# Performance work log

Hardware: AMD Instinct MI355X
Metric: run time of the kernel (lower is better)

Reference implementation:

```python
import math
import jax, jax.numpy as jnp
import numpy as np

D_MODEL = 128
NUM_HEADS = 8
FACTOR = 5


def setup_inputs() -> dict:
    key = jax.random.key(0)
    ks = jax.random.split(key, 9)
    B, L, dm = 2, 4096, D_MODEL
    s = 1.0 / math.sqrt(dm)
    return {
        "x": jax.random.normal(ks[0], (B, L, dm), dtype=jnp.float32),
        "Wq": jax.random.normal(ks[1], (dm, dm), dtype=jnp.float32) * s,
        "bq": jnp.zeros((dm,), jnp.float32),
        "Wk": jax.random.normal(ks[2], (dm, dm), dtype=jnp.float32) * s,
        "bk": jnp.zeros((dm,), jnp.float32),
        "Wv": jax.random.normal(ks[3], (dm, dm), dtype=jnp.float32) * s,
        "bv": jnp.zeros((dm,), jnp.float32),
        "Wo": jax.random.normal(ks[4], (dm, dm), dtype=jnp.float32) * s,
        "bo": jnp.zeros((dm,), jnp.float32),
    }


def reference(x, Wq, bq, Wk, bk, Wv, bv, Wo, bo):
    B, L, dm = x.shape
    H = NUM_HEADS
    D = dm // H
    inv_sqrt_d = 1.0 / math.sqrt(D)

    def split_heads(t):  # [B,L,dm] -> [B,H,L,D]
        return t.reshape(B, L, H, D).transpose(0, 2, 1, 3)

    Q = split_heads(x @ Wq + bq)
    K = split_heads(x @ Wk + bk)
    V = split_heads(x @ Wv + bv)

    # sample_k = min(L_K, int(log(L_K) * factor)); L is static under jit
    sample_k = min(L, int(math.log(L) * FACTOR))

    # _prob_QK: full scores, per-query stable exp, mean over queries, top-k keys
    scores_full = jnp.einsum("bhqd,bhkd->bhqk", Q, K) * inv_sqrt_d  # [B,H,L,L]
    m = jnp.max(scores_full, axis=-1, keepdims=True)
    e = jnp.exp(scores_full - m)
    mean_attn = jnp.mean(e, axis=2)  # [B,H,L_K]
    _, idx = jax.lax.top_k(mean_attn, sample_k)  # [B,H,sample_k]

    # gather sampled keys/values along the key axis
    Ks = jnp.take_along_axis(K, idx[..., None], axis=2)  # [B,H,s,D]
    Vs = jnp.take_along_axis(V, idx[..., None], axis=2)

    attn = jax.nn.softmax(jnp.einsum("bhqd,bhsd->bhqs", Q, Ks) * inv_sqrt_d, axis=-1)
    out = jnp.einsum("bhqs,bhsd->bhqd", attn, Vs)  # [B,H,L,D]
    out = out.transpose(0, 2, 1, 3).reshape(B, L, dm)
    return out @ Wo + bo
```

## Files before the change

### kernel.cpp

```cpp
#include <hip/hip_runtime.h>
#include <hip/hip_bf16.h>

#define L 4096
#define DM 128
#define NH 8
#define HD 16
#define NBH 16
#define SK 41
#define NSPLIT 4
#define QSCALE 0.36067376022224085f

typedef __attribute__((ext_vector_type(8))) short s16x8;
typedef __attribute__((ext_vector_type(4))) float f32x4;

__device__ __forceinline__ float bf2f(unsigned short h){ return __uint_as_float(((unsigned)h)<<16); }
__device__ __forceinline__ unsigned short f2bf(float f){
  unsigned u = __float_as_uint(f);
  u += 0x7FFFu + ((u>>16)&1u);
  return (unsigned short)(u>>16);
}
__device__ __forceinline__ float fast_exp2(float x){
  float r;
  asm("v_exp_f32 %0, %1" : "=v"(r) : "v"(x));
  return r;
}

__global__ __launch_bounds__(256) void prep(
    const float* __restrict__ x,
    const float* __restrict__ Wq, const float* __restrict__ Wk,
    const float* __restrict__ Wv, const float* __restrict__ Wo,
    unsigned short* __restrict__ Xh, unsigned short* __restrict__ Xl,
    unsigned short* __restrict__ Wph, unsigned short* __restrict__ Wpl)
{
  const int t = threadIdx.x;
  const int blk = blockIdx.x;
  if (blk < 1024){
    const long base = (long)blk*1024 + t*4;
    float4 v = *(const float4*)(x + base);
    unsigned short h[4], lo[4];
    h[0]=f2bf(v.x); lo[0]=f2bf(v.x - bf2f(h[0]));
    h[1]=f2bf(v.y); lo[1]=f2bf(v.y - bf2f(h[1]));
    h[2]=f2bf(v.z); lo[2]=f2bf(v.z - bf2f(h[2]));
    h[3]=f2bf(v.w); lo[3]=f2bf(v.w - bf2f(h[3]));
    *(uint2*)(Xh+base) = *(uint2*)h;
    *(uint2*)(Xl+base) = *(uint2*)lo;
  } else {
    const int e = (blk-1024)*256 + t;
    const int p = e >> 14;
    const int idx = e & 16383;
    const int j = idx & 7;
    const int f = idx >> 3;
    const int n = f & 127;
    const int kcg = f >> 7;
    const int k = (kcg>>1)*16 + (kcg&1)*8 + j;
    const float* W = (p==0)?Wq:((p==1)?Wk:((p==2)?Wv:Wo));
    const float v = W[k*128 + n];
    const unsigned short h = f2bf(v);
    Wph[e] = h;
    Wpl[e] = f2bf(v - bf2f(h));
  }
}

__global__ __launch_bounds__(256) void proj_mfma(
    const unsigned short* __restrict__ Xh, const unsigned short* __restrict__ Xl,
    const unsigned short* __restrict__ Wph, const unsigned short* __restrict__ Wpl,
    const float* __restrict__ bq, const float* __restrict__ bk, const float* __restrict__ bv,
    unsigned short* __restrict__ Qh, unsigned short* __restrict__ Ql,
    unsigned short* __restrict__ Kh, unsigned short* __restrict__ Kl,
    float* __restrict__ Vo)
{
  const int p = blockIdx.y;
  const float* __restrict__ bias = (p==0)?bq:((p==1)?bk:bv);
  __shared__ __align__(16) unsigned short wh[16384];
  __shared__ __align__(16) unsigned short wl[16384];
  const int t = threadIdx.x;
  {
    const uint4* gh = (const uint4*)(Wph + (long)p*16384);
    const uint4* gl = (const uint4*)(Wpl + (long)p*16384);
    uint4* sh = (uint4*)wh; uint4* sl = (uint4*)wl;
#pragma unroll
    for (int i=0;i<8;++i){ sh[t + i*256] = gh[t + i*256]; sl[t + i*256] = gl[t + i*256]; }
  }
  __syncthreads();
  const int w = t>>6, l = t&63;
  const int lc = l&15, g = l>>4;
  const int mbase = blockIdx.x*256 + w*64;
  f32x4 acc[4][8];
#pragma unroll
  for (int mt=0;mt<4;++mt)
#pragma unroll
    for (int nt=0;nt<8;++nt){ acc[mt][nt][0]=0.f; acc[mt][nt][1]=0.f; acc[mt][nt][2]=0.f; acc[mt][nt][3]=0.f; }
  const unsigned short* __restrict__ Asrc = (g<2)? Xh : Xl;
  const int koff = (g&1)*8;
  for (int kc=0; kc<8; ++kc){
    s16x8 a[4];
#pragma unroll
    for (int mt=0;mt<4;++mt)
      a[mt] = *(const s16x8*)(Asrc + ((long)(mbase + mt*16 + lc))*128 + kc*16 + koff);
#pragma unroll
    for (int nt=0;nt<8;++nt){
      const int fi = (kc*2+(g&1))*128 + nt*16 + lc;
      s16x8 b1 = ((const s16x8*)wh)[fi];
      s16x8 b2 = ((const s16x8*)wl)[fi];
#pragma unroll
      for (int mt=0;mt<4;++mt){
        acc[mt][nt] = __builtin_amdgcn_mfma_f32_16x16x32_bf16(a[mt], b1, acc[mt][nt], 0,0,0);
        acc[mt][nt] = __builtin_amdgcn_mfma_f32_16x16x32_bf16(a[mt], b2, acc[mt][nt], 0,0,0);
      }
    }
  }
#pragma unroll
  for (int nt=0;nt<8;++nt){
    const float bb = bias[nt*16 + lc];
#pragma unroll
    for (int mt=0;mt<4;++mt){
#pragma unroll
      for (int r=0;r<4;++r){
        const int row = mbase + mt*16 + g*4 + r;
        float v = acc[mt][nt][r] + bb;
        const int b = row>>12, li = row&4095;
        const long o = (((long)(b*NH + nt))*L + li)*HD + lc;
        if (p==2){
          Vo[o] = v;
        } else {
          if (p==0) v *= QSCALE;
          const unsigned short h = f2bf(v);
          const unsigned short lo2 = f2bf(v - bf2f(h));
          if (p==0){ Qh[o]=h; Ql[o]=lo2; } else { Kh[o]=h; Kl[o]=lo2; }
        }
      }
    }
  }
}

__global__ __launch_bounds__(256) void rowmax_k(
    const unsigned short* __restrict__ Qh, const unsigned short* __restrict__ Ql,
    const unsigned short* __restrict__ Kh, const unsigned short* __restrict__ Kl,
    float* __restrict__ mpart)
{
  const int bh = blockIdx.y, qt = blockIdx.x, ks = blockIdx.z;
  const int t = threadIdx.x, w = t>>6, l = t&63;
  const int half = (l>>4)&1, part = l>>5, lc = l&15;
  s16x8 aq[4];
  {
    const unsigned short* Qsrc = part ? Ql : Qh;
#pragma unroll
    for (int m=0;m<4;++m){
      const int row = qt*256 + w*64 + m*16 + lc;
      aq[m] = *(const s16x8*)(Qsrc + (((long)bh*L + row)*HD) + half*8);
    }
  }
  f32x4 fz; fz[0]=0.f; fz[1]=0.f; fz[2]=0.f; fz[3]=0.f;
  f32x4 rmax[4];
#pragma unroll
  for (int m=0;m<4;++m){ rmax[m][0]=rmax[m][1]=rmax[m][2]=rmax[m][3]=-3.4e38f; }
  const unsigned short* khp = Kh + ((long)bh*L + ks*1024 + lc)*HD + half*8;
  const unsigned short* klp = Kl + ((long)bh*L + ks*1024 + lc)*HD + half*8;
  s16x8 nb1 = *(const s16x8*)khp;
  s16x8 nb2 = *(const s16x8*)klp;
  for (int kk=0; kk<64; ++kk){
    s16x8 b1 = nb1, b2 = nb2;
    if (kk < 63){
      nb1 = *(const s16x8*)(khp + (kk+1)*16*HD);
      nb2 = *(const s16x8*)(klp + (kk+1)*16*HD);
    }
#pragma unroll
    for (int m=0;m<4;++m){
      f32x4 acc = __builtin_amdgcn_mfma_f32_16x16x32_bf16(aq[m], b2, fz, 0,0,0);
      acc = __builtin_amdgcn_mfma_f32_16x16x32_bf16(aq[m], b1, acc, 0,0,0);
#pragma unroll
      for (int r=0;r<4;++r) rmax[m][r] = fmaxf(rmax[m][r], acc[r]);
    }
  }
#pragma unroll
  for (int m=0;m<4;++m){
#pragma unroll
    for (int r=0;r<4;++r){
      float v = rmax[m][r];
      v = fmaxf(v, __shfl_xor(v, 1));
      v = fmaxf(v, __shfl_xor(v, 2));
      v = fmaxf(v, __shfl_xor(v, 4));
      v = fmaxf(v, __shfl_xor(v, 8));
      rmax[m][r] = v;
    }
  }
  if (lc == 0){
    const int q4 = l>>4;
#pragma unroll
    for (int m=0;m<4;++m){
#pragma unroll
      for (int r=0;r<4;++r){
        const int row = qt*256 + w*64 + m*16 + q4*4 + r;
        mpart[((long)ks*NBH + bh)*L + row] = rmax[m][r];
      }
    }
  }
}

__global__ __launch_bounds__(256) void mreduce(
    const float* __restrict__ mpart, float* __restrict__ wq)
{
  const int i = blockIdx.x*256 + threadIdx.x;
  float m = -3.4e38f;
#pragma unroll
  for (int p=0;p<NSPLIT;++p) m = fmaxf(m, mpart[(long)p*NBH*L + i]);
  wq[i] = fast_exp2(-m);
}

__global__ __launch_bounds__(256) void colexp_k(
    const unsigned short* __restrict__ Kh, const unsigned short* __restrict__ Kl,
    const unsigned short* __restrict__ Qh, const unsigned short* __restrict__ Ql,
    const float* __restrict__ wq, float* __restrict__ cspart)
{
  const int bh = blockIdx.y, kt = blockIdx.x, qs = blockIdx.z;
  const int t = threadIdx.x, w = t>>6, l = t&63;
  const int half = (l>>4)&1, part = l>>5, lc = l&15;
  s16x8 ak[4];
  {
    const unsigned short* Ksrc = part ? Kl : Kh;
#pragma unroll
    for (int m=0;m<4;++m){
      const int key = kt*256 + w*64 + m*16 + lc;
      ak[m] = *(const s16x8*)(Ksrc + (((long)bh*L + key)*HD) + half*8);
    }
  }
  f32x4 fz; fz[0]=0.f; fz[1]=0.f; fz[2]=0.f; fz[3]=0.f;
  f32x4 csum[4];
#pragma unroll
  for (int m=0;m<4;++m){ csum[m][0]=0.f; csum[m][1]=0.f; csum[m][2]=0.f; csum[m][3]=0.f; }
  const unsigned short* qhp = Qh + ((long)bh*L + qs*1024 + lc)*HD + half*8;
  const unsigned short* qlp = Ql + ((long)bh*L + qs*1024 + lc)*HD + half*8;
  const float* wg = wq + (long)bh*L + qs*1024 + lc;
  s16x8 nb1 = *(const s16x8*)qhp;
  s16x8 nb2 = *(const s16x8*)qlp;
  float nw = *wg;
  for (int kk=0; kk<64; ++kk){
    s16x8 b1 = nb1, b2 = nb2;
    const float wv = nw;
    if (kk < 63){
      nb1 = *(const s16x8*)(qhp + (kk+1)*16*HD);
      nb2 = *(const s16x8*)(qlp + (kk+1)*16*HD);
      nw  = wg[(kk+1)*16];
    }
#pragma unroll
    for (int m=0;m<4;++m){
      f32x4 acc = __builtin_amdgcn_mfma_f32_16x16x32_bf16(ak[m], b2, fz, 0,0,0);
      acc = __builtin_amdgcn_mfma_f32_16x16x32_bf16(ak[m], b1, acc, 0,0,0);
#pragma unroll
      for (int r=0;r<4;++r)
        csum[m][r] = fmaf(fast_exp2(acc[r]), wv, csum[m][r]);
    }
  }
#pragma unroll
  for (int m=0;m<4;++m){
#pragma unroll
    for (int r=0;r<4;++r){
      float v = csum[m][r];
      v += __shfl_xor(v, 1);
      v += __shfl_xor(v, 2);
      v += __shfl_xor(v, 4);
      v += __shfl_xor(v, 8);
      csum[m][r] = v;
    }
  }
  if (lc == 0){
    const int k4 = l>>4;
#pragma unroll
    for (int m=0;m<4;++m){
#pragma unroll
      for (int r=0;r<4;++r){
        const int key = kt*256 + w*64 + m*16 + k4*4 + r;
        cspart[((long)qs*NBH + bh)*L + key] = csum[m][r];
      }
    }
  }
}

__global__ __launch_bounds__(256) void csreduce(
    const float* __restrict__ cspart, float* __restrict__ cs)
{
  const int gid = blockIdx.x*256 + threadIdx.x;
  const long i4 = (long)gid*4;
  float4 s = {0.f,0.f,0.f,0.f};
#pragma unroll
  for (int p=0;p<NSPLIT;++p){
    float4 v = *(const float4*)(cspart + (long)p*NBH*L + i4);
    s.x += v.x; s.y += v.y; s.z += v.z; s.w += v.w;
  }
  *(float4*)(cs + i4) = s;
}

__global__ __launch_bounds__(256) void topk_gather(
    const float* __restrict__ cs,
    const unsigned short* __restrict__ Kh, const unsigned short* __restrict__ Kl,
    const float* __restrict__ V,
    float* __restrict__ Ks, float* __restrict__ Vs)
{
  const int bh = blockIdx.x;
  const int t = threadIdx.x;
  __shared__ float vals[4096];
  __shared__ unsigned hist[2048];
  __shared__ unsigned suf[256];
  __shared__ int meta[4];
  __shared__ int sel[SK];
  __shared__ int sorted[SK];
  __shared__ int tiei[4096];

  for (int i=t; i<1024; i+=256)
    *(float4*)&vals[i*4] = *(const float4*)(cs + (long)bh*L + i*4);
  __syncthreads();

  int target = SK;
  unsigned B1 = 0, P2 = 0, T = 0;
#pragma unroll
  for (int pass=0; pass<3; ++pass){
    const int nb = (pass<2) ? 2048 : 1024;
    const int chunk = nb >> 8;
    for (int i=t;i<nb;i+=256) hist[i]=0u;
    __syncthreads();
    for (int i=t;i<4096;i+=256){
      const unsigned u = __float_as_uint(vals[i]);
      bool ok; int bk;
      if (pass==0){ ok = true;              bk = (int)(u>>21); }
      else if (pass==1){ ok = ((u>>21)==B1); bk = (int)((u>>10)&0x7FFu); }
      else { ok = ((u>>10)==P2);            bk = (int)(u&0x3FFu); }
      if (ok) atomicAdd(&hist[bk], 1u);
    }
    __syncthreads();
    {
      unsigned c=0;
#pragma unroll
      for (int b=0;b<8;++b) if (b<chunk) c += hist[t*chunk+b];
      suf[t]=c;
    }
    __syncthreads();
    for (int off=1; off<256; off<<=1){
      unsigned add = (t+off<256)? suf[t+off] : 0u;
      __syncthreads();
      suf[t] += add;
      __syncthreads();
    }
    {
      const unsigned mysuf = suf[t];
      const unsigned nxt = (t==255)?0u:suf[t+1];
      if (mysuf >= (unsigned)target && nxt < (unsigned)target){
        unsigned running = nxt;
        for (int b=t*chunk+chunk-1; b>=t*chunk; --b){
          const unsigned h = hist[b];
          if (running + h >= (unsigned)target){ meta[0]=b; meta[1]=(int)running; break; }
          running += h;
        }
      }
    }
    __syncthreads();
    const unsigned B = (unsigned)meta[0];
    target -= meta[1];
    if (pass==0) B1 = B;
    else if (pass==1) P2 = (B1<<11)|B;
    else T = (P2<<10)|B;
    __syncthreads();
  }
  if (t==0){ meta[2]=0; meta[3]=0; }
  __syncthreads();
  for (int i=t;i<4096;i+=256){
    const unsigned u = __float_as_uint(vals[i]);
    if (u > T){ int p = atomicAdd(&meta[2],1); sel[p]=i; }
    else if (u == T){ int p = atomicAdd(&meta[3],1); tiei[p]=i; }
  }
  __syncthreads();
  const int ngt = meta[2];
  const int ntie = meta[3];
  for (int j=t; j<ntie; j+=256){
    const int x = tiei[j];
    int rk=0;
    for (int k=0;k<ntie;++k) rk += (tiei[k] < x);
    if (rk < target) sel[ngt+rk] = x;
  }
  __syncthreads();
  if (t<SK){
    int x=sel[t]; int rk=0;
    for (int j=0;j<SK;++j) rk += (sel[j]<x);
    sorted[rk]=x;
  }
  __syncthreads();
  for (int i=t;i<SK*HD;i+=256){
    const int j=i>>4, dd=i&15;
    const int key=sorted[j];
    const long src=((long)bh*L+key)*HD+dd;
    Ks[(long)bh*SK*HD+i]=bf2f(Kh[src])+bf2f(Kl[src]);
    Vs[(long)bh*SK*HD+i]=V[src];
  }
}

__global__ __launch_bounds__(256) void sattn(
    const unsigned short* __restrict__ Qh, const unsigned short* __restrict__ Ql,
    const float* __restrict__ Ks, const float* __restrict__ Vs,
    unsigned short* __restrict__ AOh, unsigned short* __restrict__ AOl)
{
  const int bh = blockIdx.y, qb = blockIdx.x;
  const int t = threadIdx.x;
  __shared__ float ks[SK*HD], vs[SK*HD];
  for (int i=t; i<SK*HD; i+=256){
    ks[i] = Ks[(long)bh*SK*HD + i];
    vs[i] = Vs[(long)bh*SK*HD + i];
  }
  __syncthreads();
  const int q = qb*256 + t;
  const long qo = ((long)bh*L + q)*HD;
  float qv[16];
  {
    s16x8 h0 = *(const s16x8*)(Qh+qo);
    s16x8 h1 = *(const s16x8*)(Qh+qo+8);
    s16x8 l0 = *(const s16x8*)(Ql+qo);
    s16x8 l1 = *(const s16x8*)(Ql+qo+8);
#pragma unroll
    for (int d=0; d<8; ++d){
      qv[d]   = bf2f((unsigned short)h0[d]) + bf2f((unsigned short)l0[d]);
      qv[d+8] = bf2f((unsigned short)h1[d]) + bf2f((unsigned short)l1[d]);
    }
  }
  float mrun = -3.4e38f, lrun = 0.f, out[16];
#pragma unroll
  for (int d=0; d<16; ++d) out[d] = 0.f;
  for (int j=0; j<SK; ++j){
    float4 k0 = *(const float4*)&ks[j*HD+0];
    float4 k1 = *(const float4*)&ks[j*HD+4];
    float4 k2 = *(const float4*)&ks[j*HD+8];
    float4 k3 = *(const float4*)&ks[j*HD+12];
    float s = qv[0]*k0.x;
    s = fmaf(qv[1],k0.y,s); s = fmaf(qv[2],k0.z,s); s = fmaf(qv[3],k0.w,s);
    s = fmaf(qv[4],k1.x,s); s = fmaf(qv[5],k1.y,s); s = fmaf(qv[6],k1.z,s); s = fmaf(qv[7],k1.w,s);
    s = fmaf(qv[8],k2.x,s); s = fmaf(qv[9],k2.y,s); s = fmaf(qv[10],k2.z,s); s = fmaf(qv[11],k2.w,s);
    s = fmaf(qv[12],k3.x,s); s = fmaf(qv[13],k3.y,s); s = fmaf(qv[14],k3.z,s); s = fmaf(qv[15],k3.w,s);
    if (s > mrun){
      const float c = fast_exp2(mrun - s);
      lrun *= c;
#pragma unroll
      for (int d=0; d<16; ++d) out[d] *= c;
      mrun = s;
    }
    const float p = fast_exp2(s - mrun);
    lrun += p;
    float4 v0 = *(const float4*)&vs[j*HD+0];
    float4 v1 = *(const float4*)&vs[j*HD+4];
    float4 v2 = *(const float4*)&vs[j*HD+8];
    float4 v3 = *(const float4*)&vs[j*HD+12];
    out[0]=fmaf(p,v0.x,out[0]); out[1]=fmaf(p,v0.y,out[1]); out[2]=fmaf(p,v0.z,out[2]); out[3]=fmaf(p,v0.w,out[3]);
    out[4]=fmaf(p,v1.x,out[4]); out[5]=fmaf(p,v1.y,out[5]); out[6]=fmaf(p,v1.z,out[6]); out[7]=fmaf(p,v1.w,out[7]);
    out[8]=fmaf(p,v2.x,out[8]); out[9]=fmaf(p,v2.y,out[9]); out[10]=fmaf(p,v2.z,out[10]); out[11]=fmaf(p,v2.w,out[11]);
    out[12]=fmaf(p,v3.x,out[12]); out[13]=fmaf(p,v3.y,out[13]); out[14]=fmaf(p,v3.z,out[14]); out[15]=fmaf(p,v3.w,out[15]);
  }
  const float inv = 1.f / lrun;
  const int b = bh>>3, h = bh&7;
  const long row = (long)b*L + q;
  unsigned short hv[16], lv[16];
#pragma unroll
  for (int d=0; d<16; ++d){
    const float v = out[d]*inv;
    hv[d] = f2bf(v);
    lv[d] = f2bf(v - bf2f(hv[d]));
  }
  unsigned short* oh = AOh + row*DM + h*HD;
  unsigned short* ol = AOl + row*DM + h*HD;
  *(uint4*)(oh)   = *(uint4*)(hv);
  *(uint4*)(oh+8) = *(uint4*)(hv+8);
  *(uint4*)(ol)   = *(uint4*)(lv);
  *(uint4*)(ol+8) = *(uint4*)(lv+8);
}

__global__ __launch_bounds__(256) void outproj_mfma(
    const unsigned short* __restrict__ AOh, const unsigned short* __restrict__ AOl,
    const unsigned short* __restrict__ Wph, const unsigned short* __restrict__ Wpl,
    const float* __restrict__ bo, float* __restrict__ out)
{
  __shared__ __align__(16) unsigned short wh[16384];
  __shared__ __align__(16) unsigned short wl[16384];
  const int t = threadIdx.x;
  {
    const uint4* gh = (const uint4*)(Wph + (long)3*16384);
    const uint4* gl = (const uint4*)(Wpl + (long)3*16384);
    uint4* sh = (uint4*)wh; uint4* sl = (uint4*)wl;
#pragma unroll
    for (int i=0;i<8;++i){ sh[t + i*256] = gh[t + i*256]; sl[t + i*256] = gl[t + i*256]; }
  }
  __syncthreads();
  const int w = t>>6, l = t&63;
  const int lc = l&15, g = l>>4;
  const int mbase = blockIdx.x*256 + w*64;
  f32x4 acc[4][8];
#pragma unroll
  for (int mt=0;mt<4;++mt)
#pragma unroll
    for (int nt=0;nt<8;++nt){ acc[mt][nt][0]=0.f; acc[mt][nt][1]=0.f; acc[mt][nt][2]=0.f; acc[mt][nt][3]=0.f; }
  const unsigned short* __restrict__ Asrc = (g<2)? AOh : AOl;
  const int koff = (g&1)*8;
  for (int kc=0; kc<8; ++kc){
    s16x8 a[4];
#pragma unroll
    for (int mt=0;mt<4;++mt)
      a[mt] = *(const s16x8*)(Asrc + ((long)(mbase + mt*16 + lc))*128 + kc*16 + koff);
#pragma unroll
    for (int nt=0;nt<8;++nt){
      const int fi = (kc*2+(g&1))*128 + nt*16 + lc;
      s16x8 b1 = ((const s16x8*)wh)[fi];
      s16x8 b2 = ((const s16x8*)wl)[fi];
#pragma unroll
      for (int mt=0;mt<4;++mt){
        acc[mt][nt] = __builtin_amdgcn_mfma_f32_16x16x32_bf16(a[mt], b1, acc[mt][nt], 0,0,0);
        acc[mt][nt] = __builtin_amdgcn_mfma_f32_16x16x32_bf16(a[mt], b2, acc[mt][nt], 0,0,0);
      }
    }
  }
#pragma unroll
  for (int nt=0;nt<8;++nt){
    const float bb = bo[nt*16 + lc];
#pragma unroll
    for (int mt=0;mt<4;++mt){
#pragma unroll
      for (int r=0;r<4;++r){
        const int row = mbase + mt*16 + g*4 + r;
        out[(long)row*DM + nt*16 + lc] = acc[mt][nt][r] + bb;
      }
    }
  }
}

extern "C" void kernel_launch(void* const* d_in, const int* in_sizes, int n_in,
                              void* d_out, int out_size, void* d_ws, size_t ws_size,
                              hipStream_t stream)
{
  const float* x  = (const float*)d_in[0];
  const float* Wq = (const float*)d_in[1];
  const float* bq = (const float*)d_in[2];
  const float* Wk = (const float*)d_in[3];
  const float* bk = (const float*)d_in[4];
  const float* Wv = (const float*)d_in[5];
  const float* bv = (const float*)d_in[6];
  const float* Wo = (const float*)d_in[7];
  const float* bo = (const float*)d_in[8];
  float* out = (float*)d_out;

  char* wsp = (char*)d_ws;
  size_t o = 0;
  auto alloc = [&](size_t bytes)->char*{
    char* p = wsp + o; o += (bytes + 255) & ~(size_t)255; return p;
  };
  unsigned short* Qh = (unsigned short*)alloc((size_t)NBH*L*HD*2);
  unsigned short* Ql = (unsigned short*)alloc((size_t)NBH*L*HD*2);
  unsigned short* Kh = (unsigned short*)alloc((size_t)NBH*L*HD*2);
  unsigned short* Kl = (unsigned short*)alloc((size_t)NBH*L*HD*2);
  float* Vv    = (float*)alloc((size_t)NBH*L*HD*4);
  float* mpart = (float*)alloc((size_t)NSPLIT*NBH*L*4);
  float* cspart= (float*)alloc((size_t)NSPLIT*NBH*L*4);
  float* csv   = (float*)alloc((size_t)NBH*L*4);
  float* wqv   = (float*)alloc((size_t)NBH*L*4);
  float* Ks    = (float*)alloc((size_t)NBH*SK*HD*4);
  float* Vs    = (float*)alloc((size_t)NBH*SK*HD*4);
  unsigned short* Xh  = (unsigned short*)alloc((size_t)2*L*DM*2);
  unsigned short* Xl  = (unsigned short*)alloc((size_t)2*L*DM*2);
  unsigned short* AOh = (unsigned short*)alloc((size_t)2*L*DM*2);
  unsigned short* AOl = (unsigned short*)alloc((size_t)2*L*DM*2);
  unsigned short* Wph = (unsigned short*)alloc((size_t)4*16384*2);
  unsigned short* Wpl = (unsigned short*)alloc((size_t)4*16384*2);

  prep<<<1280,256,0,stream>>>(x,Wq,Wk,Wv,Wo,Xh,Xl,Wph,Wpl);
  proj_mfma<<<dim3(32,3),256,0,stream>>>(Xh,Xl,Wph,Wpl,bq,bk,bv,Qh,Ql,Kh,Kl,Vv);
  rowmax_k<<<dim3(16,16,NSPLIT),256,0,stream>>>(Qh,Ql,Kh,Kl,mpart);
  mreduce<<<NBH*L/256,256,0,stream>>>(mpart,wqv);
  colexp_k<<<dim3(16,16,NSPLIT),256,0,stream>>>(Kh,Kl,Qh,Ql,wqv,cspart);
  csreduce<<<NBH*L/1024,256,0,stream>>>(cspart,csv);
  topk_gather<<<16,256,0,stream>>>(csv,Kh,Kl,Vv,Ks,Vs);
  sattn<<<dim3(16,16),256,0,stream>>>(Qh,Ql,Ks,Vs,AOh,AOl);
  outproj_mfma<<<32,256,0,stream>>>(AOh,AOl,Wph,Wpl,bo,out);
}
```

Baseline: 160.2 us.

## Raise parallelism across kernels and fold column-sum reduction into top-k

Doubles the key/query split count in the rowmax and colexp kernels (NSPLIT 4→8) and unrolls their loops by two with explicit double-buffered loads. Halves rows per block in the projection and output GEMMs to double their grid sizes. Splits each query across two threads in sampled attention and merges the two partial softmax states with shuffles. Removes the separate csreduce kernel by summing partials inside topk_gather, trading one launch for more reads in a 16-block kernel. The mreduce kernel (not shown) is assumed to loop over NSPLIT.

```diff
diff --git a/kernel.cpp b/kernel.cpp
--- a/kernel.cpp
+++ b/kernel.cpp
@@ -7,7 +7,9 @@
 #define HD 16
 #define NBH 16
 #define SK 41
-#define NSPLIT 4
+#define NSPLIT 8
+#define SLICE (L/NSPLIT)
+#define KK (SLICE/16)
 #define QSCALE 0.36067376022224085f
 
 typedef __attribute__((ext_vector_type(8))) short s16x8;
@@ -84,18 +86,18 @@
   __syncthreads();
   const int w = t>>6, l = t&63;
   const int lc = l&15, g = l>>4;
-  const int mbase = blockIdx.x*256 + w*64;
-  f32x4 acc[4][8];
-#pragma unroll
-  for (int mt=0;mt<4;++mt)
+  const int mbase = blockIdx.x*128 + w*32;
+  f32x4 acc[2][8];
+#pragma unroll
+  for (int mt=0;mt<2;++mt)
 #pragma unroll
     for (int nt=0;nt<8;++nt){ acc[mt][nt][0]=0.f; acc[mt][nt][1]=0.f; acc[mt][nt][2]=0.f; acc[mt][nt][3]=0.f; }
   const unsigned short* __restrict__ Asrc = (g<2)? Xh : Xl;
   const int koff = (g&1)*8;
   for (int kc=0; kc<8; ++kc){
-    s16x8 a[4];
-#pragma unroll
-    for (int mt=0;mt<4;++mt)
+    s16x8 a[2];
+#pragma unroll
+    for (int mt=0;mt<2;++mt)
       a[mt] = *(const s16x8*)(Asrc + ((long)(mbase + mt*16 + lc))*128 + kc*16 + koff);
 #pragma unroll
     for (int nt=0;nt<8;++nt){
@@ -103,7 +105,7 @@
       s16x8 b1 = ((const s16x8*)wh)[fi];
       s16x8 b2 = ((const s16x8*)wl)[fi];
 #pragma unroll
-      for (int mt=0;mt<4;++mt){
+      for (int mt=0;mt<2;++mt){
         acc[mt][nt] = __builtin_amdgcn_mfma_f32_16x16x32_bf16(a[mt], b1, acc[mt][nt], 0,0,0);
         acc[mt][nt] = __builtin_amdgcn_mfma_f32_16x16x32_bf16(a[mt], b2, acc[mt][nt], 0,0,0);
       }
@@ -113,7 +115,7 @@
   for (int nt=0;nt<8;++nt){
     const float bb = bias[nt*16 + lc];
 #pragma unroll
-    for (int mt=0;mt<4;++mt){
+    for (int mt=0;mt<2;++mt){
 #pragma unroll
       for (int r=0;r<4;++r){
         const int row = mbase + mt*16 + g*4 + r;
@@ -154,20 +156,26 @@
   f32x4 rmax[4];
 #pragma unroll
   for (int m=0;m<4;++m){ rmax[m][0]=rmax[m][1]=rmax[m][2]=rmax[m][3]=-3.4e38f; }
-  const unsigned short* khp = Kh + ((long)bh*L + ks*1024 + lc)*HD + half*8;
-  const unsigned short* klp = Kl + ((long)bh*L + ks*1024 + lc)*HD + half*8;
-  s16x8 nb1 = *(const s16x8*)khp;
-  s16x8 nb2 = *(const s16x8*)klp;
-  for (int kk=0; kk<64; ++kk){
-    s16x8 b1 = nb1, b2 = nb2;
-    if (kk < 63){
-      nb1 = *(const s16x8*)(khp + (kk+1)*16*HD);
-      nb2 = *(const s16x8*)(klp + (kk+1)*16*HD);
-    }
-#pragma unroll
-    for (int m=0;m<4;++m){
-      f32x4 acc = __builtin_amdgcn_mfma_f32_16x16x32_bf16(aq[m], b2, fz, 0,0,0);
-      acc = __builtin_amdgcn_mfma_f32_16x16x32_bf16(aq[m], b1, acc, 0,0,0);
+  const unsigned short* khp = Kh + ((long)bh*L + ks*SLICE + lc)*HD + half*8;
+  const unsigned short* klp = Kl + ((long)bh*L + ks*SLICE + lc)*HD + half*8;
+  s16x8 A1 = *(const s16x8*)khp;
+  s16x8 A2 = *(const s16x8*)klp;
+  for (int kk=0; kk<KK; kk+=2){
+    s16x8 B1 = *(const s16x8*)(khp + (kk+1)*256);
+    s16x8 B2 = *(const s16x8*)(klp + (kk+1)*256);
+#pragma unroll
+    for (int m=0;m<4;++m){
+      f32x4 acc = __builtin_amdgcn_mfma_f32_16x16x32_bf16(aq[m], A2, fz, 0,0,0);
+      acc = __builtin_amdgcn_mfma_f32_16x16x32_bf16(aq[m], A1, acc, 0,0,0);
+#pragma unroll
+      for (int r=0;r<4;++r) rmax[m][r] = fmaxf(rmax[m][r], acc[r]);
+    }
+    A1 = *(const s16x8*)(khp + (kk+2)*256);
+    A2 = *(const s16x8*)(klp + (kk+2)*256);
+#pragma unroll
+    for (int m=0;m<4;++m){
+      f32x4 acc = __builtin_amdgcn_mfma_f32_16x16x32_bf16(aq[m], B2, fz, 0,0,0);
+      acc = __builtin_amdgcn_mfma_f32_16x16x32_bf16(aq[m], B1, acc, 0,0,0);
 #pragma unroll
       for (int r=0;r<4;++r) rmax[m][r] = fmaxf(rmax[m][r], acc[r]);
     }
@@ -228,27 +236,34 @@
   f32x4 csum[4];
 #pragma unroll
   for (int m=0;m<4;++m){ csum[m][0]=0.f; csum[m][1]=0.f; csum[m][2]=0.f; csum[m][3]=0.f; }
-  const unsigned short* qhp = Qh + ((long)bh*L + qs*1024 + lc)*HD + half*8;
-  const unsigned short* qlp = Ql + ((long)bh*L + qs*1024 + lc)*HD + half*8;
-  const float* wg = wq + (long)bh*L + qs*1024 + lc;
-  s16x8 nb1 = *(const s16x8*)qhp;
-  s16x8 nb2 = *(const s16x8*)qlp;
-  float nw = *wg;
-  for (int kk=0; kk<64; ++kk){
-    s16x8 b1 = nb1, b2 = nb2;
-    const float wv = nw;
-    if (kk < 63){
-      nb1 = *(const s16x8*)(qhp + (kk+1)*16*HD);
-      nb2 = *(const s16x8*)(qlp + (kk+1)*16*HD);
-      nw  = wg[(kk+1)*16];
-    }
-#pragma unroll
-    for (int m=0;m<4;++m){
-      f32x4 acc = __builtin_amdgcn_mfma_f32_16x16x32_bf16(ak[m], b2, fz, 0,0,0);
-      acc = __builtin_amdgcn_mfma_f32_16x16x32_bf16(ak[m], b1, acc, 0,0,0);
+  const unsigned short* qhp = Qh + ((long)bh*L + qs*SLICE + lc)*HD + half*8;
+  const unsigned short* qlp = Ql + ((long)bh*L + qs*SLICE + lc)*HD + half*8;
+  const float* wg = wq + (long)bh*L + qs*SLICE + lc;
+  s16x8 A1 = *(const s16x8*)qhp;
+  s16x8 A2 = *(const s16x8*)qlp;
+  float WA = wg[0];
+  for (int kk=0; kk<KK; kk+=2){
+    s16x8 B1 = *(const s16x8*)(qhp + (kk+1)*256);
+    s16x8 B2 = *(const s16x8*)(qlp + (kk+1)*256);
+    float WB = wg[(kk+1)*16];
+#pragma unroll
+    for (int m=0;m<4;++m){
+      f32x4 acc = __builtin_amdgcn_mfma_f32_16x16x32_bf16(ak[m], A2, fz, 0,0,0);
+      acc = __builtin_amdgcn_mfma_f32_16x16x32_bf16(ak[m], A1, acc, 0,0,0);
 #pragma unroll
       for (int r=0;r<4;++r)
-        csum[m][r] = fmaf(fast_exp2(acc[r]), wv, csum[m][r]);
+        csum[m][r] = fmaf(fast_exp2(acc[r]), WA, csum[m][r]);
+    }
+    A1 = *(const s16x8*)(qhp + (kk+2)*256);
+    A2 = *(const s16x8*)(qlp + (kk+2)*256);
+    WA = wg[(kk+2)*16];
+#pragma unroll
+    for (int m=0;m<4;++m){
+      f32x4 acc = __builtin_amdgcn_mfma_f32_16x16x32_bf16(ak[m], B2, fz, 0,0,0);
+      acc = __builtin_amdgcn_mfma_f32_16x16x32_bf16(ak[m], B1, acc, 0,0,0);
+#pragma unroll
+      for (int r=0;r<4;++r)
+        csum[m][r] = fmaf(fast_exp2(acc[r]), WB, csum[m][r]);
     }
   }
 #pragma unroll
@@ -276,22 +291,8 @@
   }
 }
 
-__global__ __launch_bounds__(256) void csreduce(
-    const float* __restrict__ cspart, float* __restrict__ cs)
-{
-  const int gid = blockIdx.x*256 + threadIdx.x;
-  const long i4 = (long)gid*4;
-  float4 s = {0.f,0.f,0.f,0.f};
-#pragma unroll
-  for (int p=0;p<NSPLIT;++p){
-    float4 v = *(const float4*)(cspart + (long)p*NBH*L + i4);
-    s.x += v.x; s.y += v.y; s.z += v.z; s.w += v.w;
-  }
-  *(float4*)(cs + i4) = s;
-}
-
 __global__ __launch_bounds__(256) void topk_gather(
-    const float* __restrict__ cs,
+    const float* __restrict__ cspart,
     const unsigned short* __restrict__ Kh, const unsigned short* __restrict__ Kl,
     const float* __restrict__ V,
     float* __restrict__ Ks, float* __restrict__ Vs)
@@ -306,8 +307,15 @@
   __shared__ int sorted[SK];
   __shared__ int tiei[4096];
 
-  for (int i=t; i<1024; i+=256)
-    *(float4*)&vals[i*4] = *(const float4*)(cs + (long)bh*L + i*4);
+  for (int i=t; i<1024; i+=256){
+    float4 s = {0.f,0.f,0.f,0.f};
+#pragma unroll
+    for (int p=0;p<NSPLIT;++p){
+      float4 v = *(const float4*)(cspart + ((long)p*NBH + bh)*L + i*4);
+      s.x += v.x; s.y += v.y; s.z += v.z; s.w += v.w;
+    }
+    *(float4*)&vals[i*4] = s;
+  }
   __syncthreads();
 
   int target = SK;
@@ -405,7 +413,8 @@
     vs[i] = Vs[(long)bh*SK*HD + i];
   }
   __syncthreads();
-  const int q = qb*256 + t;
+  const int q = qb*128 + (t>>1);
+  const int half = t&1;
   const long qo = ((long)bh*L + q)*HD;
   float qv[16];
   {
@@ -422,7 +431,7 @@
   float mrun = -3.4e38f, lrun = 0.f, out[16];
 #pragma unroll
   for (int d=0; d<16; ++d) out[d] = 0.f;
-  for (int j=0; j<SK; ++j){
+  for (int j=half; j<SK; j+=2){
     float4 k0 = *(const float4*)&ks[j*HD+0];
     float4 k1 = *(const float4*)&ks[j*HD+4];
     float4 k2 = *(const float4*)&ks[j*HD+8];
@@ -450,22 +459,35 @@
     out[8]=fmaf(p,v2.x,out[8]); out[9]=fmaf(p,v2.y,out[9]); out[10]=fmaf(p,v2.z,out[10]); out[11]=fmaf(p,v2.w,out[11]);
     out[12]=fmaf(p,v3.x,out[12]); out[13]=fmaf(p,v3.y,out[13]); out[14]=fmaf(p,v3.z,out[14]); out[15]=fmaf(p,v3.w,out[15]);
   }
-  const float inv = 1.f / lrun;
-  const int b = bh>>3, h = bh&7;
-  const long row = (long)b*L + q;
-  unsigned short hv[16], lv[16];
+  const float mo = __shfl_xor(mrun, 1);
+  const float lo = __shfl_xor(lrun, 1);
+  const float mm = fmaxf(mrun, mo);
+  const float cs_ = fast_exp2(mrun - mm);
+  const float co_ = fast_exp2(mo - mm);
+  const float ltot = fmaf(lrun, cs_, lo*co_);
+  const float inv = 1.f / ltot;
 #pragma unroll
   for (int d=0; d<16; ++d){
-    const float v = out[d]*inv;
-    hv[d] = f2bf(v);
-    lv[d] = f2bf(v - bf2f(hv[d]));
-  }
-  unsigned short* oh = AOh + row*DM + h*HD;
-  unsigned short* ol = AOl + row*DM + h*HD;
-  *(uint4*)(oh)   = *(uint4*)(hv);
-  *(uint4*)(oh+8) = *(uint4*)(hv+8);
-  *(uint4*)(ol)   = *(uint4*)(lv);
-  *(uint4*)(ol+8) = *(uint4*)(lv+8);
+    const float ov = __shfl_xor(out[d], 1);
+    out[d] = fmaf(out[d]*cs_, inv, ov*co_*inv);
+  }
+  if (half == 0){
+    const int b = bh>>3, h = bh&7;
+    const long row = (long)b*L + q;
+    unsigned short hv[16], lv[16];
+#pragma unroll
+    for (int d=0; d<16; ++d){
+      const float v = out[d];
+      hv[d] = f2bf(v);
+      lv[d] = f2bf(v - bf2f(hv[d]));
+    }
+    unsigned short* oh = AOh + row*DM + h*HD;
+    unsigned short* ol = AOl + row*DM + h*HD;
+    *(uint4*)(oh)   = *(uint4*)(hv);
+    *(uint4*)(oh+8) = *(uint4*)(hv+8);
+    *(uint4*)(ol)   = *(uint4*)(lv);
+    *(uint4*)(ol+8) = *(uint4*)(lv+8);
+  }
 }
 
 __global__ __launch_bounds__(256) void outproj_mfma(
@@ -486,18 +508,18 @@
   __syncthreads();
   const int w = t>>6, l = t&63;
   const int lc = l&15, g = l>>4;
-  const int mbase = blockIdx.x*256 + w*64;
-  f32x4 acc[4][8];
-#pragma unroll
-  for (int mt=0;mt<4;++mt)
+  const int mbase = blockIdx.x*128 + w*32;
+  f32x4 acc[2][8];
+#pragma unroll
+  for (int mt=0;mt<2;++mt)
 #pragma unroll
     for (int nt=0;nt<8;++nt){ acc[mt][nt][0]=0.f; acc[mt][nt][1]=0.f; acc[mt][nt][2]=0.f; acc[mt][nt][3]=0.f; }
   const unsigned short* __restrict__ Asrc = (g<2)? AOh : AOl;
   const int koff = (g&1)*8;
   for (int kc=0; kc<8; ++kc){
-    s16x8 a[4];
-#pragma unroll
-    for (int mt=0;mt<4;++mt)
+    s16x8 a[2];
+#pragma unroll
+    for (int mt=0;mt<2;++mt)
       a[mt] = *(const s16x8*)(Asrc + ((long)(mbase + mt*16 + lc))*128 + kc*16 + koff);
 #pragma unroll
     for (int nt=0;nt<8;++nt){
@@ -505,7 +527,7 @@
       s16x8 b1 = ((const s16x8*)wh)[fi];
       s16x8 b2 = ((const s16x8*)wl)[fi];
 #pragma unroll
-      for (int mt=0;mt<4;++mt){
+      for (int mt=0;mt<2;++mt){
         acc[mt][nt] = __builtin_amdgcn_mfma_f32_16x16x32_bf16(a[mt], b1, acc[mt][nt], 0,0,0);
         acc[mt][nt] = __builtin_amdgcn_mfma_f32_16x16x32_bf16(a[mt], b2, acc[mt][nt], 0,0,0);
       }
@@ -515,7 +537,7 @@
   for (int nt=0;nt<8;++nt){
     const float bb = bo[nt*16 + lc];
 #pragma unroll
-    for (int mt=0;mt<4;++mt){
+    for (int mt=0;mt<2;++mt){
 #pragma unroll
       for (int r=0;r<4;++r){
         const int row = mbase + mt*16 + g*4 + r;
@@ -552,7 +574,6 @@
   float* Vv    = (float*)alloc((size_t)NBH*L*HD*4);
   float* mpart = (float*)alloc((size_t)NSPLIT*NBH*L*4);
   float* cspart= (float*)alloc((size_t)NSPLIT*NBH*L*4);
-  float* csv   = (float*)alloc((size_t)NBH*L*4);
   float* wqv   = (float*)alloc((size_t)NBH*L*4);
   float* Ks    = (float*)alloc((size_t)NBH*SK*HD*4);
   float* Vs    = (float*)alloc((size_t)NBH*SK*HD*4);
@@ -564,12 +585,11 @@
   unsigned short* Wpl = (unsigned short*)alloc((size_t)4*16384*2);
 
   prep<<<1280,256,0,stream>>>(x,Wq,Wk,Wv,Wo,Xh,Xl,Wph,Wpl);
-  proj_mfma<<<dim3(32,3),256,0,stream>>>(Xh,Xl,Wph,Wpl,bq,bk,bv,Qh,Ql,Kh,Kl,Vv);
+  proj_mfma<<<dim3(64,3),256,0,stream>>>(Xh,Xl,Wph,Wpl,bq,bk,bv,Qh,Ql,Kh,Kl,Vv);
   rowmax_k<<<dim3(16,16,NSPLIT),256,0,stream>>>(Qh,Ql,Kh,Kl,mpart);
   mreduce<<<NBH*L/256,256,0,stream>>>(mpart,wqv);
   colexp_k<<<dim3(16,16,NSPLIT),256,0,stream>>>(Kh,Kl,Qh,Ql,wqv,cspart);
-  csreduce<<<NBH*L/1024,256,0,stream>>>(cspart,csv);
-  topk_gather<<<16,256,0,stream>>>(csv,Kh,Kl,Vv,Ks,Vs);
-  sattn<<<dim3(16,16),256,0,stream>>>(Qh,Ql,Ks,Vs,AOh,AOl);
-  outproj_mfma<<<32,256,0,stream>>>(AOh,AOl,Wph,Wpl,bo,out);
-}
+  topk_gather<<<16,256,0,stream>>>(cspart,Kh,Kl,Vv,Ks,Vs);
+  sattn<<<dim3(32,16),256,0,stream>>>(Qh,Ql,Ks,Vs,AOh,AOl);
+  outproj_mfma<<<64,256,0,stream>>>(AOh,AOl,Wph,Wpl,bo,out);
+}
```

Result: faster. 139.7 us (-12.8%).
